# Kernel optimization log

Hardware: AMD Instinct MI355X
Metric: run time of the kernel (lower is better)

## Reference

```python
import jax, jax.numpy as jnp
import numpy as np

N_GENES = 20000   # num_all_genes
D = 256           # embedding_dim
NNZ = 640000      # nonzeros in GO adjacency (~32 avg degree)
N_COND = 2000     # number of conditions
B = 16384         # batch size
MAXG = 5          # max_genes_per_condition
L = 2             # num_gnn_layers


def setup_inputs() -> dict:
    key = jax.random.key(0)
    ks = jax.random.split(key, 12)
    cond_idx = jax.random.randint(ks[0], (B,), 0, N_COND, dtype=jnp.int32)
    pert_embedding = jax.random.normal(ks[1], (N_GENES, D), jnp.float32) * 0.05
    gnn_kernels = jax.random.normal(ks[2], (L, D, D), jnp.float32) * 0.05
    mlp_w1 = jax.random.normal(ks[3], (D, D), jnp.float32) * 0.05
    mlp_b1 = jnp.zeros((D,), jnp.float32)
    mlp_w2 = jax.random.normal(ks[4], (D, D), jnp.float32) * 0.05
    mlp_b2 = jnp.zeros((D,), jnp.float32)
    adj_row = jax.random.randint(ks[5], (NNZ,), 0, N_GENES, dtype=jnp.int64)
    adj_col = jax.random.randint(ks[6], (NNZ,), 0, N_GENES, dtype=jnp.int64)
    adj_vals = jax.random.uniform(ks[7], (NNZ,), jnp.float32)
    cond_gene_idx = jax.random.randint(ks[8], (N_COND, MAXG), 0, N_GENES, dtype=jnp.int32)
    counts = jax.random.randint(ks[9], (N_COND,), 0, MAXG + 1)
    cond_gene_mask = (jnp.arange(MAXG)[None, :] < counts[:, None]).astype(jnp.float32)
    # padded slots get -1 index like the original (later clamped to 0)
    cond_gene_idx = jnp.where(cond_gene_mask > 0, cond_gene_idx, -1)
    return {
        'cond_idx': cond_idx,
        'pert_embedding': pert_embedding,
        'gnn_kernels': gnn_kernels,
        'mlp_w1': mlp_w1, 'mlp_b1': mlp_b1,
        'mlp_w2': mlp_w2, 'mlp_b2': mlp_b2,
        'adj_row': adj_row, 'adj_col': adj_col, 'adj_vals': adj_vals,
        'cond_gene_idx': cond_gene_idx, 'cond_gene_mask': cond_gene_mask,
    }


def reference(cond_idx, pert_embedding, gnn_kernels, mlp_w1, mlp_b1,
              mlp_w2, mlp_b2, adj_row, adj_col, adj_vals,
              cond_gene_idx, cond_gene_mask):
    # --- GNN over the full gene graph (sparse adjacency @ dense emb, then dense kernel) ---
    emb = pert_embedding  # [N, D]
    for i in range(L):
        # SpMM: aggregated[r] = sum_{nnz with row r} vals * emb[col]
        msgs = adj_vals[:, None] * emb[adj_col]            # [NNZ, D]
        agg = jax.ops.segment_sum(msgs, adj_row, num_segments=N_GENES)  # [N, D]
        emb = agg @ gnn_kernels[i]                          # [N, D]
        if i < L - 1:
            emb = jax.nn.relu(emb)

    # --- per-condition gather of up to MAXG gene embeddings, masked sum ---
    gidx = cond_gene_idx[cond_idx]          # [B, MAXG] int
    gmask = cond_gene_mask[cond_idx]        # [B, MAXG]
    gidx_safe = jnp.maximum(gidx, 0)
    gene_embs = emb[gidx_safe]              # [B, MAXG, D]
    summed = jnp.sum(gene_embs * gmask[:, :, None], axis=1)  # [B, D]
    n_genes = jnp.sum(gmask, axis=1)        # [B]

    # --- small MLP (applied when n_genes > 1), identity when ==1, zeros when ==0 ---
    h = jax.nn.relu(summed @ mlp_w1 + mlp_b1)
    mlp_out = jax.nn.relu(h @ mlp_w2 + mlp_b2)  # [B, D]

    n = n_genes[:, None]
    out = jnp.where(n == 0.0, 0.0, jnp.where(n == 1.0, summed, mlp_out))
    return out
```

## Files before the change

### kernel.cpp

```cpp
#include <hip/hip_runtime.h>

static constexpr int N_GENES = 20000;
static constexpr int D       = 256;
static constexpr int NNZ     = 640000;
static constexpr int BATCH   = 16384;
static constexpr int MAXG    = 5;
static constexpr int SCAN_B  = (N_GENES + 255) / 256;

using bf16x8 = __attribute__((ext_vector_type(8))) short;
using f32x4  = __attribute__((ext_vector_type(4))) float;

__device__ __forceinline__ unsigned short f2bf(float f) {
  unsigned int u = __builtin_bit_cast(unsigned int, f);
  u += 0x7fffu + ((u >> 16) & 1u);
  return (unsigned short)(u >> 16);
}
__device__ __forceinline__ float bf2f(unsigned short h) {
  unsigned int u = ((unsigned int)h) << 16;
  return __builtin_bit_cast(float, u);
}
__device__ __forceinline__ void gload16(const void* g, void* l) {
  __builtin_amdgcn_global_load_lds(
      (const __attribute__((address_space(1))) unsigned int*)g,
      (__attribute__((address_space(3))) unsigned int*)l, 16, 0, 0);
}

__global__ void zero_int(int* __restrict__ p, int n) {
  int i = blockIdx.x * blockDim.x + threadIdx.x;
  if (i < n) p[i] = 0;
}

__global__ void count_rows(const int* __restrict__ adj_row, int* __restrict__ cnt) {
  int e = blockIdx.x * blockDim.x + threadIdx.x;
  if (e < NNZ) atomicAdd(&cnt[adj_row[e]], 1);
}

__global__ __launch_bounds__(256)
void scan_partial(const int* __restrict__ cnt, int* __restrict__ bsum) {
  __shared__ int red[256];
  int b = blockIdx.x, t = threadIdx.x, i = b * 256 + t;
  red[t] = (i < N_GENES) ? cnt[i] : 0;
  __syncthreads();
  for (int off = 128; off > 0; off >>= 1) {
    if (t < off) red[t] += red[t + off];
    __syncthreads();
  }
  if (t == 0) bsum[b] = red[0];
}

__global__ __launch_bounds__(128)
void scan_bsums(const int* __restrict__ bsum, int* __restrict__ bpre,
                int* __restrict__ total_out) {
  __shared__ int s[128];
  int t = threadIdx.x;
  int x = (t < SCAN_B) ? bsum[t] : 0;
  s[t] = x;
  __syncthreads();
  for (int off = 1; off < 128; off <<= 1) {
    int v = (t >= off) ? s[t - off] : 0;
    __syncthreads();
    s[t] += v;
    __syncthreads();
  }
  if (t < SCAN_B) bpre[t] = s[t] - x;
  if (t == SCAN_B - 1) total_out[0] = s[t];
}

__global__ __launch_bounds__(256)
void scan_final(const int* __restrict__ cnt, const int* __restrict__ bpre,
                int* __restrict__ row_ptr, int* __restrict__ fill_ctr) {
  __shared__ int s[256];
  int b = blockIdx.x, t = threadIdx.x, i = b * 256 + t;
  int x = (i < N_GENES) ? cnt[i] : 0;
  s[t] = x;
  __syncthreads();
  for (int off = 1; off < 256; off <<= 1) {
    int v = (t >= off) ? s[t - off] : 0;
    __syncthreads();
    s[t] += v;
    __syncthreads();
  }
  if (i < N_GENES) {
    int e = bpre[b] + s[t] - x;
    row_ptr[i] = e;
    fill_ctr[i] = e;
  }
}

__global__ void fill_csr(const int* __restrict__ adj_row,
                         const int* __restrict__ adj_col,
                         const float* __restrict__ vals,
                         int* __restrict__ fill_ctr, float2* __restrict__ edges) {
  int e = blockIdx.x * blockDim.x + threadIdx.x;
  if (e < NNZ) {
    int r = adj_row[e];
    int p = atomicAdd(&fill_ctr[r], 1);
    edges[p] = make_float2(__int_as_float(adj_col[e]), vals[e]);
  }
}

__global__ __launch_bounds__(256)
void conv_pert(const float* __restrict__ p, ushort4* __restrict__ o) {
  int i = blockIdx.x * 256 + threadIdx.x;
  float4 v = reinterpret_cast<const float4*>(p)[i];
  ushort4 r;
  r.x = f2bf(v.x); r.y = f2bf(v.y); r.z = f2bf(v.z); r.w = f2bf(v.w);
  o[i] = r;
}

__global__ void conv_weights(const float* __restrict__ gk, const float* __restrict__ w1,
                             const float* __restrict__ w2,
                             char* __restrict__ whi, char* __restrict__ wlo) {
  int g = blockIdx.x * 256 + threadIdx.x;
  int wid = g >> 13, rest = g & 8191;
  const float* W = (wid == 0) ? gk : (wid == 1) ? gk + 65536 : (wid == 2) ? w1 : w2;
  int c  = rest >> 9;
  int nt = c >> 2, kt = c & 3;
  int o  = (rest & 511) << 4;
  int n  = o >> 7;
  int wb = (o & 127) ^ ((n & 7) << 4);
  int k  = wb >> 1;
  size_t obase = ((size_t)wid << 17) + ((size_t)c << 13) + o;
  unsigned short* ph = (unsigned short*)(whi + obase);
  unsigned short* pl = (unsigned short*)(wlo + obase);
  #pragma unroll
  for (int e = 0; e < 8; ++e) {
    float f = W[(size_t)(kt * 64 + k + e) * 256 + nt * 64 + n];
    unsigned short h = f2bf(f);
    ph[e] = h;
    pl[e] = f2bf(f - bf2f(h));
  }
}

__global__ __launch_bounds__(256)
void spmm_csr_img(const int* __restrict__ row_ptr, const float2* __restrict__ edges,
                  const unsigned short* __restrict__ src,
                  char* __restrict__ hi_img, char* __restrict__ lo_img) {
  int row = blockIdx.x * 4 + (threadIdx.x >> 6);
  int lane = threadIdx.x & 63;
  int beg = row_ptr[row], end = row_ptr[row + 1];
  const unsigned short* sp = src + lane * 4;
  float4 acc = {0.f, 0.f, 0.f, 0.f};
  int j = beg;
  for (; j + 4 <= end; j += 4) {
    float2 d0 = edges[j], d1 = edges[j + 1], d2 = edges[j + 2], d3 = edges[j + 3];
    ushort4 g0 = *reinterpret_cast<const ushort4*>(sp + (size_t)__float_as_int(d0.x) * D);
    ushort4 g1 = *reinterpret_cast<const ushort4*>(sp + (size_t)__float_as_int(d1.x) * D);
    ushort4 g2 = *reinterpret_cast<const ushort4*>(sp + (size_t)__float_as_int(d2.x) * D);
    ushort4 g3 = *reinterpret_cast<const ushort4*>(sp + (size_t)__float_as_int(d3.x) * D);
    acc.x += d0.y * bf2f(g0.x); acc.y += d0.y * bf2f(g0.y); acc.z += d0.y * bf2f(g0.z); acc.w += d0.y * bf2f(g0.w);
    acc.x += d1.y * bf2f(g1.x); acc.y += d1.y * bf2f(g1.y); acc.z += d1.y * bf2f(g1.z); acc.w += d1.y * bf2f(g1.w);
    acc.x += d2.y * bf2f(g2.x); acc.y += d2.y * bf2f(g2.y); acc.z += d2.y * bf2f(g2.z); acc.w += d2.y * bf2f(g2.w);
    acc.x += d3.y * bf2f(g3.x); acc.y += d3.y * bf2f(g3.y); acc.z += d3.y * bf2f(g3.z); acc.w += d3.y * bf2f(g3.w);
  }
  for (; j < end; ++j) {
    float2 d = edges[j];
    ushort4 g = *reinterpret_cast<const ushort4*>(sp + (size_t)__float_as_int(d.x) * D);
    acc.x += d.y * bf2f(g.x); acc.y += d.y * bf2f(g.y); acc.z += d.y * bf2f(g.z); acc.w += d.y * bf2f(g.w);
  }
  int mt = row >> 7, r = row & 127, kt = lane >> 4;
  int wb = ((lane & 15) << 3) ^ ((r & 7) << 4);
  size_t off = ((size_t)(mt * 4 + kt) << 14) + (size_t)r * 128 + wb;
  float a4[4] = {acc.x, acc.y, acc.z, acc.w};
  ushort4 hi, lo;
  unsigned short* ph = (unsigned short*)&hi;
  unsigned short* pl = (unsigned short*)&lo;
  #pragma unroll
  for (int e = 0; e < 4; ++e) {
    unsigned short h = f2bf(a4[e]);
    ph[e] = h;
    pl[e] = f2bf(a4[e] - bf2f(h));
  }
  *reinterpret_cast<ushort4*>(hi_img + off) = hi;
  *reinterpret_cast<ushort4*>(lo_img + off) = lo;
}

__global__ __launch_bounds__(256)
void gather_conditions(const int* __restrict__ cond_idx, const int* __restrict__ cg_idx,
                       const float* __restrict__ cg_mask, const float* __restrict__ emb,
                       float* __restrict__ out, char* __restrict__ hi_img,
                       char* __restrict__ lo_img, float* __restrict__ ngenes) {
  int b = blockIdx.x * 4 + (threadIdx.x >> 6);
  int lane = threadIdx.x & 63;
  int c = cond_idx[b];
  float4 acc = {0.f, 0.f, 0.f, 0.f};
  float n = 0.f;
  #pragma unroll
  for (int g = 0; g < MAXG; ++g) {
    float m = cg_mask[c * MAXG + g];
    n += m;
    if (m > 0.f) {
      int gi = cg_idx[c * MAXG + g];
      float4 e = *reinterpret_cast<const float4*>(emb + (size_t)gi * D + lane * 4);
      acc.x += m * e.x; acc.y += m * e.y; acc.z += m * e.z; acc.w += m * e.w;
    }
  }
  *reinterpret_cast<float4*>(out + (size_t)b * D + lane * 4) = acc;
  int mt = b >> 7, r = b & 127, kt = lane >> 4;
  int wb = ((lane & 15) << 3) ^ ((r & 7) << 4);
  size_t off = ((size_t)(mt * 4 + kt) << 14) + (size_t)r * 128 + wb;
  float a4[4] = {acc.x, acc.y, acc.z, acc.w};
  ushort4 hi, lo;
  unsigned short* ph = (unsigned short*)&hi;
  unsigned short* pl = (unsigned short*)&lo;
  #pragma unroll
  for (int e = 0; e < 4; ++e) {
    unsigned short h = f2bf(a4[e]);
    ph[e] = h;
    pl[e] = f2bf(a4[e] - bf2f(h));
  }
  *reinterpret_cast<ushort4*>(hi_img + off) = hi;
  *reinterpret_cast<ushort4*>(lo_img + off) = lo;
  if (lane == 0) ngenes[b] = n;
}

enum Epi { E_F32, E_RELU_BF16, E_HIMG, E_SELECT };

template <Epi EP>
__global__ __launch_bounds__(256)
void gemm_bf16x3(const char* __restrict__ Ahi, const char* __restrict__ Alo,
                 const char* __restrict__ Bhi, const char* __restrict__ Blo,
                 const float* __restrict__ bias, float* __restrict__ C,
                 unsigned short* __restrict__ Cbf,
                 char* __restrict__ Ohi, char* __restrict__ Olo,
                 const float* __restrict__ ngenes, int M) {
  __shared__ __align__(16) char smem[49152];
  char* sAh = smem;
  char* sAl = smem + 16384;
  char* sBh = smem + 32768;
  char* sBl = smem + 40960;

  const int t  = threadIdx.x;
  const int w  = t >> 6, l = t & 63;
  const int wr = w >> 1, wc = w & 1;
  const int mt = blockIdx.y, nt = blockIdx.x;

  f32x4 acc[4][2] = {};

  const int rA = l & 15;
  const int kB = (l >> 4) << 4;
  const int xA = (rA & 7) << 4;

  for (int kt = 0; kt < 4; ++kt) {
    const char* gAh = Ahi + ((size_t)(mt * 4 + kt) << 14);
    const char* gAl = Alo + ((size_t)(mt * 4 + kt) << 14);
    const char* gBh = Bhi + ((size_t)(nt * 4 + kt) << 13);
    const char* gBl = Blo + ((size_t)(nt * 4 + kt) << 13);
    #pragma unroll
    for (int j = 0; j < 4; ++j) {
      gload16(gAh + (j * 256 + t) * 16, sAh + j * 4096 + w * 1024);
      gload16(gAl + (j * 256 + t) * 16, sAl + j * 4096 + w * 1024);
    }
    #pragma unroll
    for (int j = 0; j < 2; ++j) {
      gload16(gBh + (j * 256 + t) * 16, sBh + j * 4096 + w * 1024);
      gload16(gBl + (j * 256 + t) * 16, sBl + j * 4096 + w * 1024);
    }
    asm volatile("s_waitcnt vmcnt(0)" ::: "memory");
    __syncthreads();
    #pragma unroll
    for (int ks = 0; ks < 2; ++ks) {
      bf16x8 ah[4], al[4], bh[2], bl[2];
      #pragma unroll
      for (int i = 0; i < 4; ++i) {
        int r   = wr * 64 + i * 16 + rA;
        int off = r * 128 + ((ks * 64 + kB) ^ xA);
        ah[i] = *(const bf16x8*)(sAh + off);
        al[i] = *(const bf16x8*)(sAl + off);
      }
      #pragma unroll
      for (int j = 0; j < 2; ++j) {
        int n   = wc * 32 + j * 16 + rA;
        int off = n * 128 + ((ks * 64 + kB) ^ xA);
        bh[j] = *(const bf16x8*)(sBh + off);
        bl[j] = *(const bf16x8*)(sBl + off);
      }
      #pragma unroll
      for (int i = 0; i < 4; ++i)
        #pragma unroll
        for (int j = 0; j < 2; ++j) {
          acc[i][j] = __builtin_amdgcn_mfma_f32_16x16x32_bf16(ah[i], bh[j], acc[i][j], 0, 0, 0);
          acc[i][j] = __builtin_amdgcn_mfma_f32_16x16x32_bf16(ah[i], bl[j], acc[i][j], 0, 0, 0);
          acc[i][j] = __builtin_amdgcn_mfma_f32_16x16x32_bf16(al[i], bh[j], acc[i][j], 0, 0, 0);
        }
    }
    __syncthreads();
  }

  const int cr = (l >> 4) << 2;
  const int cc = l & 15;
  #pragma unroll
  for (int i = 0; i < 4; ++i) {
    #pragma unroll
    for (int rr = 0; rr < 4; ++rr) {
      int rin  = wr * 64 + i * 16 + cr + rr;
      int grow = mt * 128 + rin;
      if (grow >= M) continue;
      bool wr_row = true;
      if (EP == E_SELECT) wr_row = (ngenes[grow] >= 1.5f);
      #pragma unroll
      for (int j = 0; j < 2; ++j) {
        float v  = acc[i][j][rr];
        int gcol = nt * 64 + wc * 32 + j * 16 + cc;
        if (EP == E_HIMG || EP == E_SELECT) v += bias[gcol];
        if (EP != E_F32) v = fmaxf(v, 0.f);
        if (EP == E_HIMG) {
          int wb = (((gcol & 63) << 1)) ^ ((rin & 7) << 4);
          size_t off = ((size_t)(mt * 4 + nt) << 14) + (size_t)rin * 128 + wb;
          unsigned short h16 = f2bf(v);
          *(unsigned short*)(Ohi + off) = h16;
          *(unsigned short*)(Olo + off) = f2bf(v - bf2f(h16));
        } else if (EP == E_RELU_BF16) {
          Cbf[(size_t)grow * 256 + gcol] = f2bf(v);
        } else if (wr_row) {
          C[(size_t)grow * 256 + gcol] = v;
        }
      }
    }
  }
}

extern "C" void kernel_launch(void* const* d_in, const int* in_sizes, int n_in,
                              void* d_out, int out_size, void* d_ws, size_t ws_size,
                              hipStream_t stream) {
  const int*   cond_idx = (const int*)d_in[0];
  const float* pert     = (const float*)d_in[1];
  const float* gnn_k    = (const float*)d_in[2];
  const float* w1       = (const float*)d_in[3];
  const float* b1       = (const float*)d_in[4];
  const float* w2       = (const float*)d_in[5];
  const float* b2       = (const float*)d_in[6];
  const int*   adj_row  = (const int*)d_in[7];
  const int*   adj_col  = (const int*)d_in[8];
  const float* adj_vals = (const float*)d_in[9];
  const int*   cg_idx   = (const int*)d_in[10];
  const float* cg_mask  = (const float*)d_in[11];
  float* out = (float*)d_out;

  char* w = (char*)d_ws;
  auto alloc = [&](size_t bytes) {
    void* p = w;
    w += (bytes + 255) & ~size_t(255);
    return p;
  };
  constexpr int MT_G = (N_GENES + 127) / 128;
  constexpr int MT_B = BATCH / 128;
  char*   aggHi   = (char*)alloc((size_t)MT_G * 4 * 16384);
  char*   aggLo   = (char*)alloc((size_t)MT_G * 4 * 16384);
  float*  embf    = (float*)alloc((size_t)N_GENES * D * 4);
  char*   sumHi   = (char*)alloc((size_t)MT_B * 4 * 16384);
  char*   sumLo   = (char*)alloc((size_t)MT_B * 4 * 16384);
  char*   hHi     = (char*)alloc((size_t)MT_B * 4 * 16384);
  char*   hLo     = (char*)alloc((size_t)MT_B * 4 * 16384);
  char*   wHi     = (char*)alloc((size_t)4 << 17);
  char*   wLo     = (char*)alloc((size_t)4 << 17);
  float2* edges   = (float2*)alloc((size_t)NNZ * 8);
  int*    cnt     = (int*)alloc((size_t)N_GENES * 4);
  int*    row_ptr = (int*)alloc((size_t)(N_GENES + 4) * 4);
  int*    fill_ctr= (int*)alloc((size_t)N_GENES * 4);
  int*    bsum    = (int*)alloc((size_t)128 * 4);
  int*    bpre    = (int*)alloc((size_t)128 * 4);
  float*  ngenes  = (float*)alloc((size_t)BATCH * 4);

  unsigned short* pert_bf = (unsigned short*)hHi;
  unsigned short* embf_bf = (unsigned short*)embf;

  zero_int<<<(N_GENES + 255) / 256, 256, 0, stream>>>(cnt, N_GENES);
  count_rows<<<NNZ / 256, 256, 0, stream>>>(adj_row, cnt);
  scan_partial<<<SCAN_B, 256, 0, stream>>>(cnt, bsum);
  scan_bsums<<<1, 128, 0, stream>>>(bsum, bpre, row_ptr + N_GENES);
  scan_final<<<SCAN_B, 256, 0, stream>>>(cnt, bpre, row_ptr, fill_ctr);
  fill_csr<<<NNZ / 256, 256, 0, stream>>>(adj_row, adj_col, adj_vals, fill_ctr, edges);

  conv_weights<<<128, 256, 0, stream>>>(gnn_k, w1, w2, wHi, wLo);
  conv_pert<<<N_GENES * D / 4 / 256, 256, 0, stream>>>(pert, (ushort4*)pert_bf);

  spmm_csr_img<<<N_GENES / 4, 256, 0, stream>>>(row_ptr, edges, pert_bf, aggHi, aggLo);
  gemm_bf16x3<E_RELU_BF16><<<dim3(4, MT_G), 256, 0, stream>>>(
      aggHi, aggLo, wHi, wLo, nullptr, nullptr, embf_bf, nullptr, nullptr, nullptr, N_GENES);

  spmm_csr_img<<<N_GENES / 4, 256, 0, stream>>>(row_ptr, edges, embf_bf, aggHi, aggLo);
  gemm_bf16x3<E_F32><<<dim3(4, MT_G), 256, 0, stream>>>(
      aggHi, aggLo, wHi + (1 << 17), wLo + (1 << 17), nullptr, embf, nullptr, nullptr, nullptr, nullptr, N_GENES);

  gather_conditions<<<BATCH / 4, 256, 0, stream>>>(cond_idx, cg_idx, cg_mask, embf,
                                                   out, sumHi, sumLo, ngenes);

  gemm_bf16x3<E_HIMG><<<dim3(4, MT_B), 256, 0, stream>>>(
      sumHi, sumLo, wHi + (2 << 17), wLo + (2 << 17), b1, nullptr, nullptr, hHi, hLo, nullptr, BATCH);

  gemm_bf16x3<E_SELECT><<<dim3(4, MT_B), 256, 0, stream>>>(
      hHi, hLo, wHi + (3 << 17), wLo + (3 << 17), b2, out, nullptr, nullptr, nullptr, ngenes, BATCH);
}
```

Measured before the change: 333.1 us.

## Pack CSR edges to 32-bit with bf16 values, unroll SpMM by 8, widen GEMM N tile

Each CSR edge is packed into one 32-bit word (16-bit column index plus bf16 value), which halves edge-array traffic. The SpMM gather loop is unrolled to 8 edges so more loads are in flight. The GEMM block tile grows from 64 to 128 output columns, halving the grid in x and reusing each A tile across twice the columns, at the cost of 64 KB LDS and more accumulator registers. Rounding the edge weights to bf16 adds precision loss, and the 16-bit index works only because N_GENES is below 65536.

```diff
diff --git a/kernel.cpp b/kernel.cpp
--- a/kernel.cpp
+++ b/kernel.cpp
@@ -90,12 +90,12 @@
 __global__ void fill_csr(const int* __restrict__ adj_row,
                          const int* __restrict__ adj_col,
                          const float* __restrict__ vals,
-                         int* __restrict__ fill_ctr, float2* __restrict__ edges) {
+                         int* __restrict__ fill_ctr, unsigned int* __restrict__ edges) {
   int e = blockIdx.x * blockDim.x + threadIdx.x;
   if (e < NNZ) {
     int r = adj_row[e];
     int p = atomicAdd(&fill_ctr[r], 1);
-    edges[p] = make_float2(__int_as_float(adj_col[e]), vals[e]);
+    edges[p] = (unsigned int)adj_col[e] | ((unsigned int)f2bf(vals[e]) << 16);
   }
 }
 
@@ -115,7 +115,7 @@
   int wid = g >> 13, rest = g & 8191;
   const float* W = (wid == 0) ? gk : (wid == 1) ? gk + 65536 : (wid == 2) ? w1 : w2;
   int c  = rest >> 9;
-  int nt = c >> 2, kt = c & 3;
+  int nc = c >> 2, kt = c & 3;
   int o  = (rest & 511) << 4;
   int n  = o >> 7;
   int wb = (o & 127) ^ ((n & 7) << 4);
@@ -125,7 +125,7 @@
   unsigned short* pl = (unsigned short*)(wlo + obase);
   #pragma unroll
   for (int e = 0; e < 8; ++e) {
-    float f = W[(size_t)(kt * 64 + k + e) * 256 + nt * 64 + n];
+    float f = W[(size_t)(kt * 64 + k + e) * 256 + nc * 64 + n];
     unsigned short h = f2bf(f);
     ph[e] = h;
     pl[e] = f2bf(f - bf2f(h));
@@ -133,7 +133,7 @@
 }
 
 __global__ __launch_bounds__(256)
-void spmm_csr_img(const int* __restrict__ row_ptr, const float2* __restrict__ edges,
+void spmm_csr_img(const int* __restrict__ row_ptr, const unsigned int* __restrict__ edges,
                   const unsigned short* __restrict__ src,
                   char* __restrict__ hi_img, char* __restrict__ lo_img) {
   int row = blockIdx.x * 4 + (threadIdx.x >> 6);
@@ -142,21 +142,33 @@
   const unsigned short* sp = src + lane * 4;
   float4 acc = {0.f, 0.f, 0.f, 0.f};
   int j = beg;
-  for (; j + 4 <= end; j += 4) {
-    float2 d0 = edges[j], d1 = edges[j + 1], d2 = edges[j + 2], d3 = edges[j + 3];
-    ushort4 g0 = *reinterpret_cast<const ushort4*>(sp + (size_t)__float_as_int(d0.x) * D);
-    ushort4 g1 = *reinterpret_cast<const ushort4*>(sp + (size_t)__float_as_int(d1.x) * D);
-    ushort4 g2 = *reinterpret_cast<const ushort4*>(sp + (size_t)__float_as_int(d2.x) * D);
-    ushort4 g3 = *reinterpret_cast<const ushort4*>(sp + (size_t)__float_as_int(d3.x) * D);
-    acc.x += d0.y * bf2f(g0.x); acc.y += d0.y * bf2f(g0.y); acc.z += d0.y * bf2f(g0.z); acc.w += d0.y * bf2f(g0.w);
-    acc.x += d1.y * bf2f(g1.x); acc.y += d1.y * bf2f(g1.y); acc.z += d1.y * bf2f(g1.z); acc.w += d1.y * bf2f(g1.w);
-    acc.x += d2.y * bf2f(g2.x); acc.y += d2.y * bf2f(g2.y); acc.z += d2.y * bf2f(g2.z); acc.w += d2.y * bf2f(g2.w);
-    acc.x += d3.y * bf2f(g3.x); acc.y += d3.y * bf2f(g3.y); acc.z += d3.y * bf2f(g3.z); acc.w += d3.y * bf2f(g3.w);
+  for (; j + 8 <= end; j += 8) {
+    unsigned int e0 = edges[j],     e1 = edges[j + 1], e2 = edges[j + 2], e3 = edges[j + 3];
+    unsigned int e4 = edges[j + 4], e5 = edges[j + 5], e6 = edges[j + 6], e7 = edges[j + 7];
+    ushort4 g0 = *reinterpret_cast<const ushort4*>(sp + (size_t)(e0 & 0xFFFFu) * D);
+    ushort4 g1 = *reinterpret_cast<const ushort4*>(sp + (size_t)(e1 & 0xFFFFu) * D);
+    ushort4 g2 = *reinterpret_cast<const ushort4*>(sp + (size_t)(e2 & 0xFFFFu) * D);
+    ushort4 g3 = *reinterpret_cast<const ushort4*>(sp + (size_t)(e3 & 0xFFFFu) * D);
+    ushort4 g4 = *reinterpret_cast<const ushort4*>(sp + (size_t)(e4 & 0xFFFFu) * D);
+    ushort4 g5 = *reinterpret_cast<const ushort4*>(sp + (size_t)(e5 & 0xFFFFu) * D);
+    ushort4 g6 = *reinterpret_cast<const ushort4*>(sp + (size_t)(e6 & 0xFFFFu) * D);
+    ushort4 g7 = *reinterpret_cast<const ushort4*>(sp + (size_t)(e7 & 0xFFFFu) * D);
+    float v0 = bf2f(e0 >> 16), v1 = bf2f(e1 >> 16), v2 = bf2f(e2 >> 16), v3 = bf2f(e3 >> 16);
+    float v4 = bf2f(e4 >> 16), v5 = bf2f(e5 >> 16), v6 = bf2f(e6 >> 16), v7 = bf2f(e7 >> 16);
+    acc.x += v0 * bf2f(g0.x); acc.y += v0 * bf2f(g0.y); acc.z += v0 * bf2f(g0.z); acc.w += v0 * bf2f(g0.w);
+    acc.x += v1 * bf2f(g1.x); acc.y += v1 * bf2f(g1.y); acc.z += v1 * bf2f(g1.z); acc.w += v1 * bf2f(g1.w);
+    acc.x += v2 * bf2f(g2.x); acc.y += v2 * bf2f(g2.y); acc.z += v2 * bf2f(g2.z); acc.w += v2 * bf2f(g2.w);
+    acc.x += v3 * bf2f(g3.x); acc.y += v3 * bf2f(g3.y); acc.z += v3 * bf2f(g3.z); acc.w += v3 * bf2f(g3.w);
+    acc.x += v4 * bf2f(g4.x); acc.y += v4 * bf2f(g4.y); acc.z += v4 * bf2f(g4.z); acc.w += v4 * bf2f(g4.w);
+    acc.x += v5 * bf2f(g5.x); acc.y += v5 * bf2f(g5.y); acc.z += v5 * bf2f(g5.z); acc.w += v5 * bf2f(g5.w);
+    acc.x += v6 * bf2f(g6.x); acc.y += v6 * bf2f(g6.y); acc.z += v6 * bf2f(g6.z); acc.w += v6 * bf2f(g6.w);
+    acc.x += v7 * bf2f(g7.x); acc.y += v7 * bf2f(g7.y); acc.z += v7 * bf2f(g7.z); acc.w += v7 * bf2f(g7.w);
   }
   for (; j < end; ++j) {
-    float2 d = edges[j];
-    ushort4 g = *reinterpret_cast<const ushort4*>(sp + (size_t)__float_as_int(d.x) * D);
-    acc.x += d.y * bf2f(g.x); acc.y += d.y * bf2f(g.y); acc.z += d.y * bf2f(g.z); acc.w += d.y * bf2f(g.w);
+    unsigned int e = edges[j];
+    ushort4 g = *reinterpret_cast<const ushort4*>(sp + (size_t)(e & 0xFFFFu) * D);
+    float v = bf2f(e >> 16);
+    acc.x += v * bf2f(g.x); acc.y += v * bf2f(g.y); acc.z += v * bf2f(g.z); acc.w += v * bf2f(g.w);
   }
   int mt = row >> 7, r = row & 127, kt = lane >> 4;
   int wb = ((lane & 15) << 3) ^ ((r & 7) << 4);
@@ -224,28 +236,30 @@
                  unsigned short* __restrict__ Cbf,
                  char* __restrict__ Ohi, char* __restrict__ Olo,
                  const float* __restrict__ ngenes, int M) {
-  __shared__ __align__(16) char smem[49152];
+  __shared__ __align__(16) char smem[65536];
   char* sAh = smem;
   char* sAl = smem + 16384;
   char* sBh = smem + 32768;
-  char* sBl = smem + 40960;
-
-  const int t  = threadIdx.x;
-  const int w  = t >> 6, l = t & 63;
-  const int wr = w >> 1, wc = w & 1;
-  const int mt = blockIdx.y, nt = blockIdx.x;
-
-  f32x4 acc[4][2] = {};
+  char* sBl = smem + 49152;
+
+  const int t   = threadIdx.x;
+  const int w   = t >> 6, l = t & 63;
+  const int wr  = w >> 1, wc = w & 1;
+  const int mt  = blockIdx.y, nt2 = blockIdx.x;
+
+  f32x4 acc[4][4] = {};
 
   const int rA = l & 15;
   const int kB = (l >> 4) << 4;
   const int xA = (rA & 7) << 4;
 
   for (int kt = 0; kt < 4; ++kt) {
-    const char* gAh = Ahi + ((size_t)(mt * 4 + kt) << 14);
-    const char* gAl = Alo + ((size_t)(mt * 4 + kt) << 14);
-    const char* gBh = Bhi + ((size_t)(nt * 4 + kt) << 13);
-    const char* gBl = Blo + ((size_t)(nt * 4 + kt) << 13);
+    const char* gAh  = Ahi + ((size_t)(mt * 4 + kt) << 14);
+    const char* gAl  = Alo + ((size_t)(mt * 4 + kt) << 14);
+    const char* gBh0 = Bhi + ((size_t)((nt2 * 2 + 0) * 4 + kt) << 13);
+    const char* gBl0 = Blo + ((size_t)((nt2 * 2 + 0) * 4 + kt) << 13);
+    const char* gBh1 = Bhi + ((size_t)((nt2 * 2 + 1) * 4 + kt) << 13);
+    const char* gBl1 = Blo + ((size_t)((nt2 * 2 + 1) * 4 + kt) << 13);
     #pragma unroll
     for (int j = 0; j < 4; ++j) {
       gload16(gAh + (j * 256 + t) * 16, sAh + j * 4096 + w * 1024);
@@ -253,14 +267,19 @@
     }
     #pragma unroll
     for (int j = 0; j < 2; ++j) {
-      gload16(gBh + (j * 256 + t) * 16, sBh + j * 4096 + w * 1024);
-      gload16(gBl + (j * 256 + t) * 16, sBl + j * 4096 + w * 1024);
+      gload16(gBh0 + (j * 256 + t) * 16, sBh + j * 4096 + w * 1024);
+      gload16(gBl0 + (j * 256 + t) * 16, sBl + j * 4096 + w * 1024);
+    }
+    #pragma unroll
+    for (int j = 0; j < 2; ++j) {
+      gload16(gBh1 + (j * 256 + t) * 16, sBh + 8192 + j * 4096 + w * 1024);
+      gload16(gBl1 + (j * 256 + t) * 16, sBl + 8192 + j * 4096 + w * 1024);
     }
     asm volatile("s_waitcnt vmcnt(0)" ::: "memory");
     __syncthreads();
     #pragma unroll
     for (int ks = 0; ks < 2; ++ks) {
-      bf16x8 ah[4], al[4], bh[2], bl[2];
+      bf16x8 ah[4], al[4], bh[4], bl[4];
       #pragma unroll
       for (int i = 0; i < 4; ++i) {
         int r   = wr * 64 + i * 16 + rA;
@@ -269,8 +288,8 @@
         al[i] = *(const bf16x8*)(sAl + off);
       }
       #pragma unroll
-      for (int j = 0; j < 2; ++j) {
-        int n   = wc * 32 + j * 16 + rA;
+      for (int j = 0; j < 4; ++j) {
+        int n   = wc * 64 + j * 16 + rA;
         int off = n * 128 + ((ks * 64 + kB) ^ xA);
         bh[j] = *(const bf16x8*)(sBh + off);
         bl[j] = *(const bf16x8*)(sBl + off);
@@ -278,7 +297,7 @@
       #pragma unroll
       for (int i = 0; i < 4; ++i)
         #pragma unroll
-        for (int j = 0; j < 2; ++j) {
+        for (int j = 0; j < 4; ++j) {
           acc[i][j] = __builtin_amdgcn_mfma_f32_16x16x32_bf16(ah[i], bh[j], acc[i][j], 0, 0, 0);
           acc[i][j] = __builtin_amdgcn_mfma_f32_16x16x32_bf16(ah[i], bl[j], acc[i][j], 0, 0, 0);
           acc[i][j] = __builtin_amdgcn_mfma_f32_16x16x32_bf16(al[i], bh[j], acc[i][j], 0, 0, 0);
@@ -299,14 +318,17 @@
       bool wr_row = true;
       if (EP == E_SELECT) wr_row = (ngenes[grow] >= 1.5f);
       #pragma unroll
-      for (int j = 0; j < 2; ++j) {
-        float v  = acc[i][j][rr];
-        int gcol = nt * 64 + wc * 32 + j * 16 + cc;
+      for (int j = 0; j < 4; ++j) {
+        float v    = acc[i][j][rr];
+        int colin  = wc * 64 + j * 16 + cc;
+        int gcol   = nt2 * 128 + colin;
         if (EP == E_HIMG || EP == E_SELECT) v += bias[gcol];
         if (EP != E_F32) v = fmaxf(v, 0.f);
         if (EP == E_HIMG) {
-          int wb = (((gcol & 63) << 1)) ^ ((rin & 7) << 4);
-          size_t off = ((size_t)(mt * 4 + nt) << 14) + (size_t)rin * 128 + wb;
+          int kt2 = nt2 * 2 + (colin >> 6);
+          int k2  = colin & 63;
+          int wb  = (k2 << 1) ^ ((rin & 7) << 4);
+          size_t off = ((size_t)(mt * 4 + kt2) << 14) + (size_t)rin * 128 + wb;
           unsigned short h16 = f2bf(v);
           *(unsigned short*)(Ohi + off) = h16;
           *(unsigned short*)(Olo + off) = f2bf(v - bf2f(h16));
@@ -345,22 +367,22 @@
   };
   constexpr int MT_G = (N_GENES + 127) / 128;
   constexpr int MT_B = BATCH / 128;
-  char*   aggHi   = (char*)alloc((size_t)MT_G * 4 * 16384);
-  char*   aggLo   = (char*)alloc((size_t)MT_G * 4 * 16384);
-  float*  embf    = (float*)alloc((size_t)N_GENES * D * 4);
-  char*   sumHi   = (char*)alloc((size_t)MT_B * 4 * 16384);
-  char*   sumLo   = (char*)alloc((size_t)MT_B * 4 * 16384);
-  char*   hHi     = (char*)alloc((size_t)MT_B * 4 * 16384);
-  char*   hLo     = (char*)alloc((size_t)MT_B * 4 * 16384);
-  char*   wHi     = (char*)alloc((size_t)4 << 17);
-  char*   wLo     = (char*)alloc((size_t)4 << 17);
-  float2* edges   = (float2*)alloc((size_t)NNZ * 8);
-  int*    cnt     = (int*)alloc((size_t)N_GENES * 4);
-  int*    row_ptr = (int*)alloc((size_t)(N_GENES + 4) * 4);
-  int*    fill_ctr= (int*)alloc((size_t)N_GENES * 4);
-  int*    bsum    = (int*)alloc((size_t)128 * 4);
-  int*    bpre    = (int*)alloc((size_t)128 * 4);
-  float*  ngenes  = (float*)alloc((size_t)BATCH * 4);
+  char*         aggHi   = (char*)alloc((size_t)MT_G * 4 * 16384);
+  char*         aggLo   = (char*)alloc((size_t)MT_G * 4 * 16384);
+  float*        embf    = (float*)alloc((size_t)N_GENES * D * 4);
+  char*         sumHi   = (char*)alloc((size_t)MT_B * 4 * 16384);
+  char*         sumLo   = (char*)alloc((size_t)MT_B * 4 * 16384);
+  char*         hHi     = (char*)alloc((size_t)MT_B * 4 * 16384);
+  char*         hLo     = (char*)alloc((size_t)MT_B * 4 * 16384);
+  char*         wHi     = (char*)alloc((size_t)4 << 17);
+  char*         wLo     = (char*)alloc((size_t)4 << 17);
+  unsigned int* edges   = (unsigned int*)alloc((size_t)NNZ * 4);
+  int*          cnt     = (int*)alloc((size_t)N_GENES * 4);
+  int*          row_ptr = (int*)alloc((size_t)(N_GENES + 4) * 4);
+  int*          fill_ctr= (int*)alloc((size_t)N_GENES * 4);
+  int*          bsum    = (int*)alloc((size_t)128 * 4);
+  int*          bpre    = (int*)alloc((size_t)128 * 4);
+  float*        ngenes  = (float*)alloc((size_t)BATCH * 4);
 
   unsigned short* pert_bf = (unsigned short*)hHi;
   unsigned short* embf_bf = (unsigned short*)embf;
@@ -376,19 +398,19 @@
   conv_pert<<<N_GENES * D / 4 / 256, 256, 0, stream>>>(pert, (ushort4*)pert_bf);
 
   spmm_csr_img<<<N_GENES / 4, 256, 0, stream>>>(row_ptr, edges, pert_bf, aggHi, aggLo);
-  gemm_bf16x3<E_RELU_BF16><<<dim3(4, MT_G), 256, 0, stream>>>(
+  gemm_bf16x3<E_RELU_BF16><<<dim3(2, MT_G), 256, 0, stream>>>(
       aggHi, aggLo, wHi, wLo, nullptr, nullptr, embf_bf, nullptr, nullptr, nullptr, N_GENES);
 
   spmm_csr_img<<<N_GENES / 4, 256, 0, stream>>>(row_ptr, edges, embf_bf, aggHi, aggLo);
-  gemm_bf16x3<E_F32><<<dim3(4, MT_G), 256, 0, stream>>>(
+  gemm_bf16x3<E_F32><<<dim3(2, MT_G), 256, 0, stream>>>(
       aggHi, aggLo, wHi + (1 << 17), wLo + (1 << 17), nullptr, embf, nullptr, nullptr, nullptr, nullptr, N_GENES);
 
   gather_conditions<<<BATCH / 4, 256, 0, stream>>>(cond_idx, cg_idx, cg_mask, embf,
                                                    out, sumHi, sumLo, ngenes);
 
-  gemm_bf16x3<E_HIMG><<<dim3(4, MT_B), 256, 0, stream>>>(
+  gemm_bf16x3<E_HIMG><<<dim3(2, MT_B), 256, 0, stream>>>(
       sumHi, sumLo, wHi + (2 << 17), wLo + (2 << 17), b1, nullptr, nullptr, hHi, hLo, nullptr, BATCH);
 
-  gemm_bf16x3<E_SELECT><<<dim3(4, MT_B), 256, 0, stream>>>(
+  gemm_bf16x3<E_SELECT><<<dim3(2, MT_B), 256, 0, stream>>>(
       hHi, hLo, wHi + (3 << 17), wLo + (3 << 17), b2, out, nullptr, nullptr, nullptr, ngenes, BATCH);
 }
```

Measured after the change: 329.9 us. No clear change (-1.0%).
